# Kernel tuning notes

Measured on AMD Instinct MI355X. Metric: run time of the kernel, lower is better.

Reference implementation:

```python
import jax, jax.numpy as jnp
import numpy as np
import math

N_HEADS = 8

def setup_inputs() -> dict:
    key = jax.random.key(0)
    qkv = jax.random.normal(key, (2, 1536, 4096), dtype=jnp.float32)
    return {"qkv": qkv}

def reference(qkv):
    bs, width, length = qkv.shape
    ch = width // (3 * N_HEADS)
    # [bs*H, 3*ch, T] -> split into q, k, v each [bs*H, ch, T]
    qkv_r = qkv.reshape(bs * N_HEADS, 3 * ch, length)
    q, k, v = jnp.split(qkv_r, 3, axis=1)
    scale = 1.0 / math.sqrt(math.sqrt(ch))
    # scores [b, t, s]
    weight = jnp.einsum('bct,bcs->bts', q * scale, k * scale)
    weight = jax.nn.softmax(weight.astype(jnp.float32), axis=-1).astype(weight.dtype)
    a = jnp.einsum('bts,bcs->bct', weight, v)
    return a.reshape(bs, N_HEADS * ch, length)
```

## Files before the change

kernel.cpp:

```cpp
#include <hip/hip_runtime.h>

#define TSEQ 4096
#define QB   128
#define KB   64
#define NT   (TSEQ / KB)

typedef __attribute__((ext_vector_type(16))) float f32x16;
typedef __attribute__((ext_vector_type(8)))  short bf16x8;
typedef __attribute__((ext_vector_type(4)))  unsigned uint4v;

union Frag { unsigned u[4]; bf16x8 v; };

static __device__ __forceinline__ unsigned cvt_pk(float lo, float hi) {
  unsigned r;
  asm("v_cvt_pk_bf16_f32 %0, %1, %2" : "=v"(r) : "v"(lo), "v"(hi));
  return r;
}

static __device__ __forceinline__ void gload16(const void* g, void* l) {
  __builtin_amdgcn_global_load_lds(
      (const __attribute__((address_space(1))) unsigned*)g,
      (__attribute__((address_space(3))) unsigned*)l, 16, 0, 0);
}

__global__ __launch_bounds__(256)
void preconvert_kernel(const float* __restrict__ qkv,
                       unsigned short* __restrict__ kimg,
                       unsigned short* __restrict__ vimg) {
  const int tile = blockIdx.x & 63;
  const int bh   = blockIdx.x >> 6;
  const int bsI  = bh >> 3;
  const int head = bh & 7;
  const size_t base = ((size_t)bsI * 1536 + (size_t)head * 192) * TSEQ;
  const float* __restrict__ Kg = qkv + base + (size_t)64  * TSEQ;
  const float* __restrict__ Vg = qkv + base + (size_t)128 * TSEQ;
  const int s0 = tile * KB;
  const int t  = threadIdx.x;
  const size_t tb = (size_t)(bh * 64 + tile) * 8192;

  {
    const int s = t & 63;
    char* kout = (char*)kimg + tb + (size_t)s * 128;
    const unsigned swz = (unsigned)((s & 7) << 4);
#pragma unroll
    for (int q = 0; q < 2; ++q) {
      const int cc = (t >> 6) + q * 4;
      float f[8];
#pragma unroll
      for (int j = 0; j < 8; ++j)
        f[j] = Kg[(size_t)(8 * cc + j) * TSEQ + s0 + s];
      uint4v d = { cvt_pk(f[0], f[1]), cvt_pk(f[2], f[3]),
                   cvt_pk(f[4], f[5]), cvt_pk(f[6], f[7]) };
      *(uint4v*)(kout + (((unsigned)(cc << 4)) ^ swz)) = d;
    }
  }

  {
    const int c  = t >> 2;
    const int sb = (t & 3) * 16;
    const float* src = &Vg[(size_t)c * TSEQ + s0 + sb];
    const float4 a0 = ((const float4*)src)[0];
    const float4 a1 = ((const float4*)src)[1];
    const float4 a2 = ((const float4*)src)[2];
    const float4 a3 = ((const float4*)src)[3];
    char* vout = (char*)vimg + tb + (size_t)c * 128;
    const unsigned cswz = (unsigned)((c & 7) << 4);
    const int ss = (t & 3) * 2;
    uint4v d0 = { cvt_pk(a0.x, a0.y), cvt_pk(a0.z, a0.w),
                  cvt_pk(a1.x, a1.y), cvt_pk(a1.z, a1.w) };
    uint4v d1 = { cvt_pk(a2.x, a2.y), cvt_pk(a2.z, a2.w),
                  cvt_pk(a3.x, a3.y), cvt_pk(a3.z, a3.w) };
    *(uint4v*)(vout + (((unsigned)(ss << 4)) ^ cswz))       = d0;
    *(uint4v*)(vout + (((unsigned)((ss + 1) << 4)) ^ cswz)) = d1;
  }
}

__global__ __launch_bounds__(256, 2)
void qkv_attn_kernel(const float* __restrict__ qkv,
                     const unsigned short* __restrict__ kimg,
                     const unsigned short* __restrict__ vimg,
                     float* __restrict__ out) {
  __shared__ __align__(16) unsigned short Kt[2][KB * 64];
  __shared__ __align__(16) unsigned short Vt[2][64 * KB];

  const int tid  = threadIdx.x;
  const int w    = tid >> 6;
  const int lane = tid & 63;
  const int h    = lane >> 5;
  const int ln   = lane & 31;

  const int bid  = blockIdx.x;
  const int qt   = bid & 31;
  const int bh   = bid >> 5;
  const int bsI  = bh >> 3;
  const int head = bh & 7;

  const size_t base = ((size_t)bsI * 1536 + (size_t)head * 192) * TSEQ;
  const float* __restrict__ Qg = qkv + base;

  const int tq = qt * QB + w * 32 + ln;

  const float QSCALE = 0.125f * 1.44269504088896340736f;

  Frag qf[4];
#pragma unroll
  for (int ks = 0; ks < 4; ++ks) {
#pragma unroll
    for (int p = 0; p < 4; ++p) {
      const int c = ks * 16 + h * 8 + 2 * p;
      const float a = Qg[(size_t)c * TSEQ + tq] * QSCALE;
      const float b = Qg[(size_t)(c + 1) * TSEQ + tq] * QSCALE;
      qf[ks].u[p] = cvt_pk(a, b);
    }
  }

  f32x16 acc0 = {0,0,0,0,0,0,0,0,0,0,0,0,0,0,0,0};
  f32x16 acc1 = {0,0,0,0,0,0,0,0,0,0,0,0,0,0,0,0};
  float lrun = 0.0f;

  const size_t hb = (size_t)bh * 64 * 8192;
  const char* __restrict__ kim = (const char*)kimg + hb + w * 2048 + lane * 16;
  const char* __restrict__ vim = (const char*)vimg + hb + w * 2048 + lane * 16;

#define STAGE(buf, tile)                                                    \
  {                                                                         \
    const size_t o = (size_t)(tile) * 8192;                                 \
    char* kl = (char*)(&Kt[buf][0]) + w * 2048;                             \
    char* vl = (char*)(&Vt[buf][0]) + w * 2048;                             \
    gload16(kim + o, kl);                                                   \
    gload16(kim + o + 1024, kl + 1024);                                     \
    gload16(vim + o, vl);                                                   \
    gload16(vim + o + 1024, vl + 1024);                                     \
  }

  STAGE(0, 0);

  for (int it = 0; it < NT; ++it) {
    const int cur = it & 1;

    if (it + 1 < NT) {
      STAGE(cur ^ 1, it + 1);
      asm volatile("s_waitcnt vmcnt(4)" ::: "memory");
    } else {
      asm volatile("s_waitcnt vmcnt(0)" ::: "memory");
    }
    __builtin_amdgcn_s_barrier();
    __builtin_amdgcn_sched_barrier(0);

    const char* kbase = (const char*)(&Kt[cur][0]);
    const char* vbase = (const char*)(&Vt[cur][0]);

    f32x16 sc0 = {0,0,0,0,0,0,0,0,0,0,0,0,0,0,0,0};
    f32x16 sc1 = {0,0,0,0,0,0,0,0,0,0,0,0,0,0,0,0};
    __builtin_amdgcn_s_setprio(1);
#pragma unroll
    for (int ks = 0; ks < 4; ++ks) {
      const int coff2 = (ks * 16 + h * 8) * 2;
      const int sA = ln, sB = 32 + ln;
      const bf16x8 kA = *(const bf16x8*)(kbase + sA * 128 + (coff2 ^ ((sA & 7) << 4)));
      const bf16x8 kB = *(const bf16x8*)(kbase + sB * 128 + (coff2 ^ ((sB & 7) << 4)));
      sc0 = __builtin_amdgcn_mfma_f32_32x32x16_bf16(kA, qf[ks].v, sc0, 0, 0, 0);
      sc1 = __builtin_amdgcn_mfma_f32_32x32x16_bf16(kB, qf[ks].v, sc1, 0, 0, 0);
    }
    __builtin_amdgcn_s_setprio(0);

    float ssum = 0.0f;
#pragma unroll
    for (int r = 0; r < 16; ++r) {
      const float p0 = __builtin_amdgcn_exp2f(sc0[r]);
      const float p1 = __builtin_amdgcn_exp2f(sc1[r]);
      sc0[r] = p0; sc1[r] = p1;
      ssum += p0 + p1;
    }
    ssum += __shfl_xor(ssum, 32);
    lrun += ssum;

    Frag pf[4];
#pragma unroll
    for (int mt = 0; mt < 2; ++mt) {
      const f32x16& s = mt ? sc1 : sc0;
      unsigned A0 = cvt_pk(s[0],  s[1]),  A1 = cvt_pk(s[2],  s[3]);
      unsigned B0 = cvt_pk(s[4],  s[5]),  B1 = cvt_pk(s[6],  s[7]);
      unsigned C0 = cvt_pk(s[8],  s[9]),  C1 = cvt_pk(s[10], s[11]);
      unsigned D0 = cvt_pk(s[12], s[13]), D1 = cvt_pk(s[14], s[15]);
      asm("v_permlane32_swap_b32 %0, %1" : "+v"(A0), "+v"(B0));
      asm("v_permlane32_swap_b32 %0, %1" : "+v"(A1), "+v"(B1));
      asm("v_permlane32_swap_b32 %0, %1" : "+v"(C0), "+v"(D0));
      asm("v_permlane32_swap_b32 %0, %1" : "+v"(C1), "+v"(D1));
      pf[2 * mt + 0].u[0] = A0; pf[2 * mt + 0].u[1] = A1;
      pf[2 * mt + 0].u[2] = B0; pf[2 * mt + 0].u[3] = B1;
      pf[2 * mt + 1].u[0] = C0; pf[2 * mt + 1].u[1] = C1;
      pf[2 * mt + 1].u[2] = D0; pf[2 * mt + 1].u[3] = D1;
    }

    __builtin_amdgcn_s_setprio(1);
#pragma unroll
    for (int ks = 0; ks < 4; ++ks) {
      const int soff2 = (ks * 16 + h * 8) * 2;
      const int cA = ln, cB = 32 + ln;
      const bf16x8 vA = *(const bf16x8*)(vbase + cA * 128 + (soff2 ^ ((cA & 7) << 4)));
      const bf16x8 vB = *(const bf16x8*)(vbase + cB * 128 + (soff2 ^ ((cB & 7) << 4)));
      acc0 = __builtin_amdgcn_mfma_f32_32x32x16_bf16(vA, pf[ks].v, acc0, 0, 0, 0);
      acc1 = __builtin_amdgcn_mfma_f32_32x32x16_bf16(vB, pf[ks].v, acc1, 0, 0, 0);
    }
    __builtin_amdgcn_s_setprio(0);

    __builtin_amdgcn_sched_barrier(0);
    __builtin_amdgcn_s_barrier();
  }

  const float linv = 1.0f / lrun;
  const size_t obase = ((size_t)bsI * 512 + (size_t)head * 64) * TSEQ + tq;
#pragma unroll
  for (int r = 0; r < 16; ++r) {
    const int crow = (r & 3) + 8 * (r >> 2) + 4 * h;
    out[obase + (size_t)crow * TSEQ]        = acc0[r] * linv;
    out[obase + (size_t)(crow + 32) * TSEQ] = acc1[r] * linv;
  }
}

extern "C" void kernel_launch(void* const* d_in, const int* in_sizes, int n_in,
                              void* d_out, int out_size, void* d_ws, size_t ws_size,
                              hipStream_t stream) {
  const float* qkv = (const float*)d_in[0];
  float* out = (float*)d_out;
  (void)in_sizes; (void)n_in; (void)out_size; (void)ws_size;

  unsigned short* kimg = (unsigned short*)d_ws;
  unsigned short* vimg = (unsigned short*)((char*)d_ws + 8388608);

  hipLaunchKernelGGL(preconvert_kernel, dim3(16 * 64), dim3(256), 0, stream,
                     qkv, kimg, vimg);
  hipLaunchKernelGGL(qkv_attn_kernel, dim3(16 * (TSEQ / QB)), dim3(256), 0,
                     stream, qkv, kimg, vimg, out);
}
```

Measured before the change: 102.8 us.

## Double key tile to 128 and remap blocks so each head stays on one XCD

Raises the key/value tile from 64 to 128, which halves the main-loop iterations and their barriers and gives each wave four independent score MFMAs and eight PV MFMAs per tile. Both kernels now decode block IDs so that all blocks of a given batch-head land on the same XCD, keeping that head's K/V images in one L2. The K/V staging is also issued before the Q fragment loads, so the first tile fetch overlaps the Q conversion. In exchange, LDS use per block doubles and register pressure rises (four score accumulators and eight P fragments), which may limit the two-blocks-per-CU occupancy.

```diff
diff --git a/kernel.cpp b/kernel.cpp
--- a/kernel.cpp
+++ b/kernel.cpp
@@ -2,7 +2,7 @@
 
 #define TSEQ 4096
 #define QB   128
-#define KB   64
+#define KB   128
 #define NT   (TSEQ / KB)
 
 typedef __attribute__((ext_vector_type(16))) float f32x16;
@@ -23,12 +23,18 @@
       (__attribute__((address_space(3))) unsigned*)l, 16, 0, 0);
 }
 
+static __device__ __forceinline__ void decode_bid(int hw, int& bh, int& sub) {
+  const int xcd = hw & 7, slot = hw >> 3;
+  bh  = xcd * 2 + (slot >> 5);
+  sub = slot & 31;
+}
+
 __global__ __launch_bounds__(256)
 void preconvert_kernel(const float* __restrict__ qkv,
                        unsigned short* __restrict__ kimg,
                        unsigned short* __restrict__ vimg) {
-  const int tile = blockIdx.x & 63;
-  const int bh   = blockIdx.x >> 6;
+  int bh, tile;
+  decode_bid(blockIdx.x, bh, tile);
   const int bsI  = bh >> 3;
   const int head = bh & 7;
   const size_t base = ((size_t)bsI * 1536 + (size_t)head * 192) * TSEQ;
@@ -36,15 +42,15 @@
   const float* __restrict__ Vg = qkv + base + (size_t)128 * TSEQ;
   const int s0 = tile * KB;
   const int t  = threadIdx.x;
-  const size_t tb = (size_t)(bh * 64 + tile) * 8192;
+  const size_t tb = (size_t)(bh * NT + tile) * 16384;
 
   {
-    const int s = t & 63;
+    const int s = t & 127;
     char* kout = (char*)kimg + tb + (size_t)s * 128;
     const unsigned swz = (unsigned)((s & 7) << 4);
 #pragma unroll
-    for (int q = 0; q < 2; ++q) {
-      const int cc = (t >> 6) + q * 4;
+    for (int q = 0; q < 4; ++q) {
+      const int cc = (t >> 7) * 4 + q;
       float f[8];
 #pragma unroll
       for (int j = 0; j < 8; ++j)
@@ -56,22 +62,18 @@
   }
 
   {
-    const int c  = t >> 2;
-    const int sb = (t & 3) * 16;
-    const float* src = &Vg[(size_t)c * TSEQ + s0 + sb];
-    const float4 a0 = ((const float4*)src)[0];
-    const float4 a1 = ((const float4*)src)[1];
-    const float4 a2 = ((const float4*)src)[2];
-    const float4 a3 = ((const float4*)src)[3];
-    char* vout = (char*)vimg + tb + (size_t)c * 128;
+    const int c = t >> 2;
+    char* vout = (char*)vimg + tb + (size_t)c * 256;
     const unsigned cswz = (unsigned)((c & 7) << 4);
-    const int ss = (t & 3) * 2;
-    uint4v d0 = { cvt_pk(a0.x, a0.y), cvt_pk(a0.z, a0.w),
-                  cvt_pk(a1.x, a1.y), cvt_pk(a1.z, a1.w) };
-    uint4v d1 = { cvt_pk(a2.x, a2.y), cvt_pk(a2.z, a2.w),
-                  cvt_pk(a3.x, a3.y), cvt_pk(a3.z, a3.w) };
-    *(uint4v*)(vout + (((unsigned)(ss << 4)) ^ cswz))       = d0;
-    *(uint4v*)(vout + (((unsigned)((ss + 1) << 4)) ^ cswz)) = d1;
+#pragma unroll
+    for (int q = 0; q < 4; ++q) {
+      const int ss = (t & 3) * 4 + q;
+      const float4 a0 = ((const float4*)&Vg[(size_t)c * TSEQ + s0 + 8 * ss])[0];
+      const float4 a1 = ((const float4*)&Vg[(size_t)c * TSEQ + s0 + 8 * ss])[1];
+      uint4v d = { cvt_pk(a0.x, a0.y), cvt_pk(a0.z, a0.w),
+                   cvt_pk(a1.x, a1.y), cvt_pk(a1.z, a1.w) };
+      *(uint4v*)(vout + (((unsigned)(ss << 4)) ^ cswz)) = d;
+    }
   }
 }
 
@@ -89,9 +91,8 @@
   const int h    = lane >> 5;
   const int ln   = lane & 31;
 
-  const int bid  = blockIdx.x;
-  const int qt   = bid & 31;
-  const int bh   = bid >> 5;
+  int bh, qt;
+  decode_bid(blockIdx.x, bh, qt);
   const int bsI  = bh >> 3;
   const int head = bh & 7;
 
@@ -101,6 +102,27 @@
   const int tq = qt * QB + w * 32 + ln;
 
   const float QSCALE = 0.125f * 1.44269504088896340736f;
+
+  const size_t hb = (size_t)bh * NT * 16384;
+  const char* __restrict__ kim = (const char*)kimg + hb + w * 4096 + lane * 16;
+  const char* __restrict__ vim = (const char*)vimg + hb + w * 4096 + lane * 16;
+
+#define STAGE(buf, tile)                                                    \
+  {                                                                         \
+    const size_t o = (size_t)(tile) * 16384;                                \
+    char* kl = (char*)(&Kt[buf][0]) + w * 4096;                             \
+    char* vl = (char*)(&Vt[buf][0]) + w * 4096;                             \
+    gload16(kim + o,        kl);                                            \
+    gload16(kim + o + 1024, kl + 1024);                                     \
+    gload16(kim + o + 2048, kl + 2048);                                     \
+    gload16(kim + o + 3072, kl + 3072);                                     \
+    gload16(vim + o,        vl);                                            \
+    gload16(vim + o + 1024, vl + 1024);                                     \
+    gload16(vim + o + 2048, vl + 2048);                                     \
+    gload16(vim + o + 3072, vl + 3072);                                     \
+  }
+
+  STAGE(0, 0);
 
   Frag qf[4];
 #pragma unroll
@@ -118,29 +140,14 @@
   f32x16 acc1 = {0,0,0,0,0,0,0,0,0,0,0,0,0,0,0,0};
   float lrun = 0.0f;
 
-  const size_t hb = (size_t)bh * 64 * 8192;
-  const char* __restrict__ kim = (const char*)kimg + hb + w * 2048 + lane * 16;
-  const char* __restrict__ vim = (const char*)vimg + hb + w * 2048 + lane * 16;
-
-#define STAGE(buf, tile)                                                    \
-  {                                                                         \
-    const size_t o = (size_t)(tile) * 8192;                                 \
-    char* kl = (char*)(&Kt[buf][0]) + w * 2048;                             \
-    char* vl = (char*)(&Vt[buf][0]) + w * 2048;                             \
-    gload16(kim + o, kl);                                                   \
-    gload16(kim + o + 1024, kl + 1024);                                     \
-    gload16(vim + o, vl);                                                   \
-    gload16(vim + o + 1024, vl + 1024);                                     \
-  }
-
-  STAGE(0, 0);
+  const unsigned lswz = (unsigned)((ln & 7) << 4);
 
   for (int it = 0; it < NT; ++it) {
     const int cur = it & 1;
 
     if (it + 1 < NT) {
       STAGE(cur ^ 1, it + 1);
-      asm volatile("s_waitcnt vmcnt(4)" ::: "memory");
+      asm volatile("s_waitcnt vmcnt(8)" ::: "memory");
     } else {
       asm volatile("s_waitcnt vmcnt(0)" ::: "memory");
     }
@@ -150,35 +157,39 @@
     const char* kbase = (const char*)(&Kt[cur][0]);
     const char* vbase = (const char*)(&Vt[cur][0]);
 
-    f32x16 sc0 = {0,0,0,0,0,0,0,0,0,0,0,0,0,0,0,0};
-    f32x16 sc1 = {0,0,0,0,0,0,0,0,0,0,0,0,0,0,0,0};
+    f32x16 sc[4];
+#pragma unroll
+    for (int m = 0; m < 4; ++m) sc[m] = (f32x16){0,0,0,0,0,0,0,0,0,0,0,0,0,0,0,0};
     __builtin_amdgcn_s_setprio(1);
 #pragma unroll
     for (int ks = 0; ks < 4; ++ks) {
-      const int coff2 = (ks * 16 + h * 8) * 2;
-      const int sA = ln, sB = 32 + ln;
-      const bf16x8 kA = *(const bf16x8*)(kbase + sA * 128 + (coff2 ^ ((sA & 7) << 4)));
-      const bf16x8 kB = *(const bf16x8*)(kbase + sB * 128 + (coff2 ^ ((sB & 7) << 4)));
-      sc0 = __builtin_amdgcn_mfma_f32_32x32x16_bf16(kA, qf[ks].v, sc0, 0, 0, 0);
-      sc1 = __builtin_amdgcn_mfma_f32_32x32x16_bf16(kB, qf[ks].v, sc1, 0, 0, 0);
+      const unsigned coffx = ((unsigned)(32 * ks + 16 * h)) ^ lswz;
+#pragma unroll
+      for (int m = 0; m < 4; ++m) {
+        const int row = 32 * m + ln;
+        const bf16x8 kf = *(const bf16x8*)(kbase + row * 128 + coffx);
+        sc[m] = __builtin_amdgcn_mfma_f32_32x32x16_bf16(kf, qf[ks].v, sc[m], 0, 0, 0);
+      }
     }
     __builtin_amdgcn_s_setprio(0);
 
     float ssum = 0.0f;
 #pragma unroll
-    for (int r = 0; r < 16; ++r) {
-      const float p0 = __builtin_amdgcn_exp2f(sc0[r]);
-      const float p1 = __builtin_amdgcn_exp2f(sc1[r]);
-      sc0[r] = p0; sc1[r] = p1;
-      ssum += p0 + p1;
+    for (int m = 0; m < 4; ++m) {
+#pragma unroll
+      for (int r = 0; r < 16; ++r) {
+        const float p = __builtin_amdgcn_exp2f(sc[m][r]);
+        sc[m][r] = p;
+        ssum += p;
+      }
     }
     ssum += __shfl_xor(ssum, 32);
     lrun += ssum;
 
-    Frag pf[4];
-#pragma unroll
-    for (int mt = 0; mt < 2; ++mt) {
-      const f32x16& s = mt ? sc1 : sc0;
+    Frag pf[8];
+#pragma unroll
+    for (int m = 0; m < 4; ++m) {
+      const f32x16& s = sc[m];
       unsigned A0 = cvt_pk(s[0],  s[1]),  A1 = cvt_pk(s[2],  s[3]);
       unsigned B0 = cvt_pk(s[4],  s[5]),  B1 = cvt_pk(s[6],  s[7]);
       unsigned C0 = cvt_pk(s[8],  s[9]),  C1 = cvt_pk(s[10], s[11]);
@@ -187,19 +198,18 @@
       asm("v_permlane32_swap_b32 %0, %1" : "+v"(A1), "+v"(B1));
       asm("v_permlane32_swap_b32 %0, %1" : "+v"(C0), "+v"(D0));
       asm("v_permlane32_swap_b32 %0, %1" : "+v"(C1), "+v"(D1));
-      pf[2 * mt + 0].u[0] = A0; pf[2 * mt + 0].u[1] = A1;
-      pf[2 * mt + 0].u[2] = B0; pf[2 * mt + 0].u[3] = B1;
-      pf[2 * mt + 1].u[0] = C0; pf[2 * mt + 1].u[1] = C1;
-      pf[2 * mt + 1].u[2] = D0; pf[2 * mt + 1].u[3] = D1;
+      pf[2 * m + 0].u[0] = A0; pf[2 * m + 0].u[1] = A1;
+      pf[2 * m + 0].u[2] = B0; pf[2 * m + 0].u[3] = B1;
+      pf[2 * m + 1].u[0] = C0; pf[2 * m + 1].u[1] = C1;
+      pf[2 * m + 1].u[2] = D0; pf[2 * m + 1].u[3] = D1;
     }
 
     __builtin_amdgcn_s_setprio(1);
 #pragma unroll
-    for (int ks = 0; ks < 4; ++ks) {
-      const int soff2 = (ks * 16 + h * 8) * 2;
-      const int cA = ln, cB = 32 + ln;
-      const bf16x8 vA = *(const bf16x8*)(vbase + cA * 128 + (soff2 ^ ((cA & 7) << 4)));
-      const bf16x8 vB = *(const bf16x8*)(vbase + cB * 128 + (soff2 ^ ((cB & 7) << 4)));
+    for (int ks = 0; ks < 8; ++ks) {
+      const unsigned soffx = ((unsigned)(32 * ks + 16 * h)) ^ lswz;
+      const bf16x8 vA = *(const bf16x8*)(vbase + ln * 256 + soffx);
+      const bf16x8 vB = *(const bf16x8*)(vbase + (32 + ln) * 256 + soffx);
       acc0 = __builtin_amdgcn_mfma_f32_32x32x16_bf16(vA, pf[ks].v, acc0, 0, 0, 0);
       acc1 = __builtin_amdgcn_mfma_f32_32x32x16_bf16(vB, pf[ks].v, acc1, 0, 0, 0);
     }
@@ -229,7 +239,7 @@
   unsigned short* kimg = (unsigned short*)d_ws;
   unsigned short* vimg = (unsigned short*)((char*)d_ws + 8388608);
 
-  hipLaunchKernelGGL(preconvert_kernel, dim3(16 * 64), dim3(256), 0, stream,
+  hipLaunchKernelGGL(preconvert_kernel, dim3(16 * NT), dim3(256), 0, stream,
                      qkv, kimg, vimg);
   hipLaunchKernelGGL(qkv_attn_kernel, dim3(16 * (TSEQ / QB)), dim3(256), 0,
                      stream, qkv, kimg, vimg, out);
```

Result: faster. 99.52 us (-3.2%).

## Split key sequence across two wave groups per block and remap blocks per XCD

Applied to the files above, without the earlier changes.

Each attention block now has 512 threads in two groups of four waves. Each group walks half of the key/value tiles with its own double-buffered LDS slots, and at the end the partial accumulators and row sums are merged through LDS before writing. Block indices are remapped so that all blocks of one batch-head land on the same XCD, for both the preconvert and attention kernels, to improve L2 reuse of the bf16 K/V images. The aim is more waves in flight and a shorter serial loop per wave. The cost is a doubled LDS footprint per block, an extra reduction pass through shared memory, and half the threads idle during the output store.

```diff
diff --git a/kernel.cpp b/kernel.cpp
--- a/kernel.cpp
+++ b/kernel.cpp
@@ -3,7 +3,8 @@
 #define TSEQ 4096
 #define QB   128
 #define KB   64
-#define NT   (TSEQ / KB)
+#define NTT  (TSEQ / KB)
+#define NTG  (NTT / 2)
 
 typedef __attribute__((ext_vector_type(16))) float f32x16;
 typedef __attribute__((ext_vector_type(8)))  short bf16x8;
@@ -23,12 +24,23 @@
       (__attribute__((address_space(3))) unsigned*)l, 16, 0, 0);
 }
 
+static __device__ __forceinline__ void decode_attn(int hw, int& bh, int& sub) {
+  const int xcd = hw & 7, slot = hw >> 3;
+  bh  = xcd * 2 + (slot >> 5);
+  sub = slot & 31;
+}
+static __device__ __forceinline__ void decode_pre(int hw, int& bh, int& sub) {
+  const int xcd = hw & 7, slot = hw >> 3;
+  bh  = xcd * 2 + (slot >> 6);
+  sub = slot & 63;
+}
+
 __global__ __launch_bounds__(256)
 void preconvert_kernel(const float* __restrict__ qkv,
                        unsigned short* __restrict__ kimg,
                        unsigned short* __restrict__ vimg) {
-  const int tile = blockIdx.x & 63;
-  const int bh   = blockIdx.x >> 6;
+  int bh, tile;
+  decode_pre(blockIdx.x, bh, tile);
   const int bsI  = bh >> 3;
   const int head = bh & 7;
   const size_t base = ((size_t)bsI * 1536 + (size_t)head * 192) * TSEQ;
@@ -36,7 +48,7 @@
   const float* __restrict__ Vg = qkv + base + (size_t)128 * TSEQ;
   const int s0 = tile * KB;
   const int t  = threadIdx.x;
-  const size_t tb = (size_t)(bh * 64 + tile) * 8192;
+  const size_t tb = (size_t)(bh * NTT + tile) * 8192;
 
   {
     const int s = t & 63;
@@ -75,32 +87,50 @@
   }
 }
 
-__global__ __launch_bounds__(256, 2)
+__global__ __launch_bounds__(512, 4)
 void qkv_attn_kernel(const float* __restrict__ qkv,
                      const unsigned short* __restrict__ kimg,
                      const unsigned short* __restrict__ vimg,
                      float* __restrict__ out) {
-  __shared__ __align__(16) unsigned short Kt[2][KB * 64];
-  __shared__ __align__(16) unsigned short Vt[2][64 * KB];
+  __shared__ __align__(16) unsigned short Kt[2][2][KB * 64];
+  __shared__ __align__(16) unsigned short Vt[2][2][64 * KB];
 
   const int tid  = threadIdx.x;
   const int w    = tid >> 6;
+  const int g    = w >> 2;
+  const int wg   = w & 3;
   const int lane = tid & 63;
   const int h    = lane >> 5;
   const int ln   = lane & 31;
 
-  const int bid  = blockIdx.x;
-  const int qt   = bid & 31;
-  const int bh   = bid >> 5;
+  int bh, qt;
+  decode_attn(blockIdx.x, bh, qt);
   const int bsI  = bh >> 3;
   const int head = bh & 7;
 
   const size_t base = ((size_t)bsI * 1536 + (size_t)head * 192) * TSEQ;
   const float* __restrict__ Qg = qkv + base;
 
-  const int tq = qt * QB + w * 32 + ln;
+  const int tq = qt * QB + wg * 32 + ln;
 
   const float QSCALE = 0.125f * 1.44269504088896340736f;
+
+  const size_t hb = (size_t)bh * NTT * 8192;
+  const char* __restrict__ kim = (const char*)kimg + hb + wg * 2048 + lane * 16;
+  const char* __restrict__ vim = (const char*)vimg + hb + wg * 2048 + lane * 16;
+
+#define STAGE(buf, tile)                                                    \
+  {                                                                         \
+    const size_t o = (size_t)(g * NTG + (tile)) * 8192;                     \
+    char* kl = (char*)(&Kt[g][buf][0]) + wg * 2048;                         \
+    char* vl = (char*)(&Vt[g][buf][0]) + wg * 2048;                         \
+    gload16(kim + o, kl);                                                   \
+    gload16(kim + o + 1024, kl + 1024);                                    \
+    gload16(vim + o, vl);                                                   \
+    gload16(vim + o + 1024, vl + 1024);                                    \
+  }
+
+  STAGE(0, 0);
 
   Frag qf[4];
 #pragma unroll
@@ -118,27 +148,10 @@
   f32x16 acc1 = {0,0,0,0,0,0,0,0,0,0,0,0,0,0,0,0};
   float lrun = 0.0f;
 
-  const size_t hb = (size_t)bh * 64 * 8192;
-  const char* __restrict__ kim = (const char*)kimg + hb + w * 2048 + lane * 16;
-  const char* __restrict__ vim = (const char*)vimg + hb + w * 2048 + lane * 16;
-
-#define STAGE(buf, tile)                                                    \
-  {                                                                         \
-    const size_t o = (size_t)(tile) * 8192;                                 \
-    char* kl = (char*)(&Kt[buf][0]) + w * 2048;                             \
-    char* vl = (char*)(&Vt[buf][0]) + w * 2048;                             \
-    gload16(kim + o, kl);                                                   \
-    gload16(kim + o + 1024, kl + 1024);                                     \
-    gload16(vim + o, vl);                                                   \
-    gload16(vim + o + 1024, vl + 1024);                                     \
-  }
-
-  STAGE(0, 0);
-
-  for (int it = 0; it < NT; ++it) {
+  for (int it = 0; it < NTG; ++it) {
     const int cur = it & 1;
 
-    if (it + 1 < NT) {
+    if (it + 1 < NTG) {
       STAGE(cur ^ 1, it + 1);
       asm volatile("s_waitcnt vmcnt(4)" ::: "memory");
     } else {
@@ -147,8 +160,8 @@
     __builtin_amdgcn_s_barrier();
     __builtin_amdgcn_sched_barrier(0);
 
-    const char* kbase = (const char*)(&Kt[cur][0]);
-    const char* vbase = (const char*)(&Vt[cur][0]);
+    const char* kbase = (const char*)(&Kt[g][cur][0]);
+    const char* vbase = (const char*)(&Vt[g][cur][0]);
 
     f32x16 sc0 = {0,0,0,0,0,0,0,0,0,0,0,0,0,0,0,0};
     f32x16 sc1 = {0,0,0,0,0,0,0,0,0,0,0,0,0,0,0,0};
@@ -209,13 +222,31 @@
     __builtin_amdgcn_s_barrier();
   }
 
-  const float linv = 1.0f / lrun;
-  const size_t obase = ((size_t)bsI * 512 + (size_t)head * 64) * TSEQ + tq;
-#pragma unroll
-  for (int r = 0; r < 16; ++r) {
-    const int crow = (r & 3) + 8 * (r >> 2) + 4 * h;
-    out[obase + (size_t)crow * TSEQ]        = acc0[r] * linv;
-    out[obase + (size_t)(crow + 32) * TSEQ] = acc1[r] * linv;
+  float* exch0 = (float*)(&Kt[0][0][0]);
+  float* exch1 = (float*)(&Vt[0][0][0]);
+  float* lex   = (float*)((char*)(&Vt[0][0][0]) + 20480);
+  const int t0 = tid & 255;
+
+  if (g == 1) {
+#pragma unroll
+    for (int r = 0; r < 16; ++r) {
+      exch0[t0 * 17 + r] = acc0[r];
+      exch1[t0 * 17 + r] = acc1[r];
+    }
+    lex[t0] = lrun;
+  }
+  __syncthreads();
+  if (g == 0) {
+    const float linv = 1.0f / (lrun + lex[t0]);
+    const size_t obase = ((size_t)bsI * 512 + (size_t)head * 64) * TSEQ + tq;
+#pragma unroll
+    for (int r = 0; r < 16; ++r) {
+      const int crow = (r & 3) + 8 * (r >> 2) + 4 * h;
+      out[obase + (size_t)crow * TSEQ] =
+          (acc0[r] + exch0[t0 * 17 + r]) * linv;
+      out[obase + (size_t)(crow + 32) * TSEQ] =
+          (acc1[r] + exch1[t0 * 17 + r]) * linv;
+    }
   }
 }
 
@@ -229,8 +260,8 @@
   unsigned short* kimg = (unsigned short*)d_ws;
   unsigned short* vimg = (unsigned short*)((char*)d_ws + 8388608);
 
-  hipLaunchKernelGGL(preconvert_kernel, dim3(16 * 64), dim3(256), 0, stream,
+  hipLaunchKernelGGL(preconvert_kernel, dim3(16 * NTT), dim3(256), 0, stream,
                      qkv, kimg, vimg);
-  hipLaunchKernelGGL(qkv_attn_kernel, dim3(16 * (TSEQ / QB)), dim3(256), 0,
+  hipLaunchKernelGGL(qkv_attn_kernel, dim3(16 * (TSEQ / QB)), dim3(512), 0,
                      stream, qkv, kimg, vimg, out);
 }
```

Measured after the change: 94.41 us. 1.09x faster.

## Split keys across waves with per-wave LDS buffers and cross-wave reduction

Applied to the files above, without the earlier changes.

Each block now owns 64 queries instead of 128. Its four waves each take a quarter of the key range with private double-buffered LDS, so the per-iteration block barriers go away. Each wave computes two 32-query tiles that share every K/V fragment load, and the K/V images are re-tiled into 32-key chunks. At the end, partial accumulators and row sums are reduced through LDS. Block IDs are also remapped to group heads across XCDs. The trade-offs are more LDS use, a final reduction, twice as many blocks, and higher register pressure from four accumulators.

```diff
diff --git a/kernel.cpp b/kernel.cpp
--- a/kernel.cpp
+++ b/kernel.cpp
@@ -1,9 +1,6 @@
 #include <hip/hip_runtime.h>
 
 #define TSEQ 4096
-#define QB   128
-#define KB   64
-#define NT   (TSEQ / KB)
 
 typedef __attribute__((ext_vector_type(16))) float f32x16;
 typedef __attribute__((ext_vector_type(8)))  short bf16x8;
@@ -27,51 +24,40 @@
 void preconvert_kernel(const float* __restrict__ qkv,
                        unsigned short* __restrict__ kimg,
                        unsigned short* __restrict__ vimg) {
-  const int tile = blockIdx.x & 63;
-  const int bh   = blockIdx.x >> 6;
+  const int hw   = blockIdx.x;
+  const int slot = hw >> 3;
+  const int bh   = (hw & 7) * 2 + (slot >> 7);
+  const int tile = slot & 127;
   const int bsI  = bh >> 3;
   const int head = bh & 7;
   const size_t base = ((size_t)bsI * 1536 + (size_t)head * 192) * TSEQ;
   const float* __restrict__ Kg = qkv + base + (size_t)64  * TSEQ;
   const float* __restrict__ Vg = qkv + base + (size_t)128 * TSEQ;
-  const int s0 = tile * KB;
+  const int s0 = tile * 32;
   const int t  = threadIdx.x;
-  const size_t tb = (size_t)(bh * 64 + tile) * 8192;
+  const size_t tb = (size_t)(bh * 128 + tile) * 4096;
 
   {
-    const int s = t & 63;
-    char* kout = (char*)kimg + tb + (size_t)s * 128;
-    const unsigned swz = (unsigned)((s & 7) << 4);
-#pragma unroll
-    for (int q = 0; q < 2; ++q) {
-      const int cc = (t >> 6) + q * 4;
-      float f[8];
-#pragma unroll
-      for (int j = 0; j < 8; ++j)
-        f[j] = Kg[(size_t)(8 * cc + j) * TSEQ + s0 + s];
-      uint4v d = { cvt_pk(f[0], f[1]), cvt_pk(f[2], f[3]),
-                   cvt_pk(f[4], f[5]), cvt_pk(f[6], f[7]) };
-      *(uint4v*)(kout + (((unsigned)(cc << 4)) ^ swz)) = d;
-    }
+    const int s = t & 31, cc = t >> 5;
+    float f[8];
+#pragma unroll
+    for (int j = 0; j < 8; ++j)
+      f[j] = Kg[(size_t)(8 * cc + j) * TSEQ + s0 + s];
+    uint4v d = { cvt_pk(f[0], f[1]), cvt_pk(f[2], f[3]),
+                 cvt_pk(f[4], f[5]), cvt_pk(f[6], f[7]) };
+    *(uint4v*)((char*)kimg + tb + (size_t)s * 128 +
+               (((unsigned)(cc << 4)) ^ ((unsigned)((s & 7) << 4)))) = d;
   }
 
   {
-    const int c  = t >> 2;
-    const int sb = (t & 3) * 16;
-    const float* src = &Vg[(size_t)c * TSEQ + s0 + sb];
+    const int c = t >> 2, ss = t & 3;
+    const float* src = &Vg[(size_t)c * TSEQ + s0 + 8 * ss];
     const float4 a0 = ((const float4*)src)[0];
     const float4 a1 = ((const float4*)src)[1];
-    const float4 a2 = ((const float4*)src)[2];
-    const float4 a3 = ((const float4*)src)[3];
-    char* vout = (char*)vimg + tb + (size_t)c * 128;
-    const unsigned cswz = (unsigned)((c & 7) << 4);
-    const int ss = (t & 3) * 2;
-    uint4v d0 = { cvt_pk(a0.x, a0.y), cvt_pk(a0.z, a0.w),
-                  cvt_pk(a1.x, a1.y), cvt_pk(a1.z, a1.w) };
-    uint4v d1 = { cvt_pk(a2.x, a2.y), cvt_pk(a2.z, a2.w),
-                  cvt_pk(a3.x, a3.y), cvt_pk(a3.z, a3.w) };
-    *(uint4v*)(vout + (((unsigned)(ss << 4)) ^ cswz))       = d0;
-    *(uint4v*)(vout + (((unsigned)((ss + 1) << 4)) ^ cswz)) = d1;
+    uint4v d = { cvt_pk(a0.x, a0.y), cvt_pk(a0.z, a0.w),
+                 cvt_pk(a1.x, a1.y), cvt_pk(a1.z, a1.w) };
+    *(uint4v*)((char*)vimg + tb + (size_t)c * 64 +
+               (((unsigned)(ss << 4)) ^ ((unsigned)((c & 3) << 4)))) = d;
   }
 }
 
@@ -80,8 +66,7 @@
                      const unsigned short* __restrict__ kimg,
                      const unsigned short* __restrict__ vimg,
                      float* __restrict__ out) {
-  __shared__ __align__(16) unsigned short Kt[2][KB * 64];
-  __shared__ __align__(16) unsigned short Vt[2][64 * KB];
+  __shared__ __align__(16) char lds[65536];
 
   const int tid  = threadIdx.x;
   const int w    = tid >> 6;
@@ -89,96 +74,118 @@
   const int h    = lane >> 5;
   const int ln   = lane & 31;
 
-  const int bid  = blockIdx.x;
-  const int qt   = bid & 31;
-  const int bh   = bid >> 5;
-  const int bsI  = bh >> 3;
-  const int head = bh & 7;
+  const int hw    = blockIdx.x;
+  const int slot  = hw >> 3;
+  const int bh    = (hw & 7) * 2 + (slot >> 6);
+  const int qslot = slot & 63;
+  const int bsI   = bh >> 3;
+  const int head  = bh & 7;
 
   const size_t base = ((size_t)bsI * 1536 + (size_t)head * 192) * TSEQ;
   const float* __restrict__ Qg = qkv + base;
-
-  const int tq = qt * QB + w * 32 + ln;
+  const int q0 = qslot * 64;
 
   const float QSCALE = 0.125f * 1.44269504088896340736f;
 
-  Frag qf[4];
+  char* kbuf0 = lds + w * 16384;
+  char* kbuf1 = kbuf0 + 4096;
+  char* vbuf0 = kbuf0 + 8192;
+  char* vbuf1 = kbuf0 + 12288;
+
+  const char* kim = (const char*)kimg + ((size_t)bh * 128 + w * 32) * 4096 + lane * 16;
+  const char* vim = (const char*)vimg + ((size_t)bh * 128 + w * 32) * 4096 + lane * 16;
+
+#define STAGE(kb, vb, it)                                                   \
+  {                                                                         \
+    const char* ks_ = kim + (size_t)(it) * 4096;                            \
+    const char* vs_ = vim + (size_t)(it) * 4096;                            \
+    gload16(ks_,        kb);                                                \
+    gload16(ks_ + 1024, (char*)(kb) + 1024);                                \
+    gload16(ks_ + 2048, (char*)(kb) + 2048);                                \
+    gload16(ks_ + 3072, (char*)(kb) + 3072);                                \
+    gload16(vs_,        vb);                                                \
+    gload16(vs_ + 1024, (char*)(vb) + 1024);                                \
+    gload16(vs_ + 2048, (char*)(vb) + 2048);                                \
+    gload16(vs_ + 3072, (char*)(vb) + 3072);                                \
+  }
+
+  STAGE(kbuf0, vbuf0, 0);
+
+  Frag qf0[4], qf1[4];
 #pragma unroll
   for (int ks = 0; ks < 4; ++ks) {
 #pragma unroll
     for (int p = 0; p < 4; ++p) {
       const int c = ks * 16 + h * 8 + 2 * p;
-      const float a = Qg[(size_t)c * TSEQ + tq] * QSCALE;
-      const float b = Qg[(size_t)(c + 1) * TSEQ + tq] * QSCALE;
-      qf[ks].u[p] = cvt_pk(a, b);
-    }
-  }
-
-  f32x16 acc0 = {0,0,0,0,0,0,0,0,0,0,0,0,0,0,0,0};
-  f32x16 acc1 = {0,0,0,0,0,0,0,0,0,0,0,0,0,0,0,0};
-  float lrun = 0.0f;
-
-  const size_t hb = (size_t)bh * 64 * 8192;
-  const char* __restrict__ kim = (const char*)kimg + hb + w * 2048 + lane * 16;
-  const char* __restrict__ vim = (const char*)vimg + hb + w * 2048 + lane * 16;
-
-#define STAGE(buf, tile)                                                    \
-  {                                                                         \
-    const size_t o = (size_t)(tile) * 8192;                                 \
-    char* kl = (char*)(&Kt[buf][0]) + w * 2048;                             \
-    char* vl = (char*)(&Vt[buf][0]) + w * 2048;                             \
-    gload16(kim + o, kl);                                                   \
-    gload16(kim + o + 1024, kl + 1024);                                     \
-    gload16(vim + o, vl);                                                   \
-    gload16(vim + o + 1024, vl + 1024);                                     \
-  }
-
-  STAGE(0, 0);
-
-  for (int it = 0; it < NT; ++it) {
+      const float a0 = Qg[(size_t)c * TSEQ + q0 + ln] * QSCALE;
+      const float b0 = Qg[(size_t)(c + 1) * TSEQ + q0 + ln] * QSCALE;
+      const float a1 = Qg[(size_t)c * TSEQ + q0 + 32 + ln] * QSCALE;
+      const float b1 = Qg[(size_t)(c + 1) * TSEQ + q0 + 32 + ln] * QSCALE;
+      qf0[ks].u[p] = cvt_pk(a0, b0);
+      qf1[ks].u[p] = cvt_pk(a1, b1);
+    }
+  }
+
+  int koff[4], voff[2][2];
+#pragma unroll
+  for (int ks = 0; ks < 4; ++ks) {
+    const int off2 = (ks * 16 + h * 8) * 2;
+    koff[ks] = ln * 128 + (off2 ^ ((ln & 7) << 4));
+  }
+#pragma unroll
+  for (int ks2 = 0; ks2 < 2; ++ks2) {
+    const int ss = ks2 * 2 + h;
+    voff[ks2][0] = ln * 64        + (((unsigned)(ss << 4)) ^ ((ln & 3) << 4));
+    voff[ks2][1] = (32 + ln) * 64 + (((unsigned)(ss << 4)) ^ ((ln & 3) << 4));
+  }
+
+  f32x16 zv = {0,0,0,0,0,0,0,0,0,0,0,0,0,0,0,0};
+  asm("" : "+v"(zv));
+
+  f32x16 acc00 = zv, acc01 = zv, acc10 = zv, acc11 = zv;
+  float lr0 = 0.0f, lr1 = 0.0f;
+
+  for (int it = 0; it < 32; ++it) {
     const int cur = it & 1;
-
-    if (it + 1 < NT) {
-      STAGE(cur ^ 1, it + 1);
-      asm volatile("s_waitcnt vmcnt(4)" ::: "memory");
+    char* kb = cur ? kbuf1 : kbuf0;
+    char* vb = cur ? vbuf1 : vbuf0;
+
+    if (it + 1 < 32) {
+      STAGE(cur ? kbuf0 : kbuf1, cur ? vbuf0 : vbuf1, it + 1);
+      asm volatile("s_waitcnt vmcnt(8)" ::: "memory");
     } else {
       asm volatile("s_waitcnt vmcnt(0)" ::: "memory");
     }
-    __builtin_amdgcn_s_barrier();
     __builtin_amdgcn_sched_barrier(0);
 
-    const char* kbase = (const char*)(&Kt[cur][0]);
-    const char* vbase = (const char*)(&Vt[cur][0]);
-
-    f32x16 sc0 = {0,0,0,0,0,0,0,0,0,0,0,0,0,0,0,0};
-    f32x16 sc1 = {0,0,0,0,0,0,0,0,0,0,0,0,0,0,0,0};
-    __builtin_amdgcn_s_setprio(1);
-#pragma unroll
-    for (int ks = 0; ks < 4; ++ks) {
-      const int coff2 = (ks * 16 + h * 8) * 2;
-      const int sA = ln, sB = 32 + ln;
-      const bf16x8 kA = *(const bf16x8*)(kbase + sA * 128 + (coff2 ^ ((sA & 7) << 4)));
-      const bf16x8 kB = *(const bf16x8*)(kbase + sB * 128 + (coff2 ^ ((sB & 7) << 4)));
-      sc0 = __builtin_amdgcn_mfma_f32_32x32x16_bf16(kA, qf[ks].v, sc0, 0, 0, 0);
-      sc1 = __builtin_amdgcn_mfma_f32_32x32x16_bf16(kB, qf[ks].v, sc1, 0, 0, 0);
-    }
-    __builtin_amdgcn_s_setprio(0);
-
-    float ssum = 0.0f;
+    f32x16 sc0, sc1;
+    {
+      const bf16x8 kA = *(const bf16x8*)(kb + koff[0]);
+      sc0 = __builtin_amdgcn_mfma_f32_32x32x16_bf16(kA, qf0[0].v, zv, 0, 0, 0);
+      sc1 = __builtin_amdgcn_mfma_f32_32x32x16_bf16(kA, qf1[0].v, zv, 0, 0, 0);
+    }
+#pragma unroll
+    for (int ks = 1; ks < 4; ++ks) {
+      const bf16x8 kA = *(const bf16x8*)(kb + koff[ks]);
+      sc0 = __builtin_amdgcn_mfma_f32_32x32x16_bf16(kA, qf0[ks].v, sc0, 0, 0, 0);
+      sc1 = __builtin_amdgcn_mfma_f32_32x32x16_bf16(kA, qf1[ks].v, sc1, 0, 0, 0);
+    }
+
+    float ls0 = 0.0f, ls1 = 0.0f;
 #pragma unroll
     for (int r = 0; r < 16; ++r) {
       const float p0 = __builtin_amdgcn_exp2f(sc0[r]);
       const float p1 = __builtin_amdgcn_exp2f(sc1[r]);
       sc0[r] = p0; sc1[r] = p1;
-      ssum += p0 + p1;
-    }
-    ssum += __shfl_xor(ssum, 32);
-    lrun += ssum;
-
-    Frag pf[4];
-#pragma unroll
-    for (int mt = 0; mt < 2; ++mt) {
-      const f32x16& s = mt ? sc1 : sc0;
+      ls0 += p0; ls1 += p1;
+    }
+    lr0 += ls0; lr1 += ls1;
+
+    Frag pf0[2], pf1[2];
+#pragma unroll
+    for (int nb = 0; nb < 2; ++nb) {
+      const f32x16& s = nb ? sc1 : sc0;
+      Frag* pf = nb ? pf1 : pf0;
       unsigned A0 = cvt_pk(s[0],  s[1]),  A1 = cvt_pk(s[2],  s[3]);
       unsigned B0 = cvt_pk(s[4],  s[5]),  B1 = cvt_pk(s[6],  s[7]);
       unsigned C0 = cvt_pk(s[8],  s[9]),  C1 = cvt_pk(s[10], s[11]);
@@ -187,35 +194,60 @@
       asm("v_permlane32_swap_b32 %0, %1" : "+v"(A1), "+v"(B1));
       asm("v_permlane32_swap_b32 %0, %1" : "+v"(C0), "+v"(D0));
       asm("v_permlane32_swap_b32 %0, %1" : "+v"(C1), "+v"(D1));
-      pf[2 * mt + 0].u[0] = A0; pf[2 * mt + 0].u[1] = A1;
-      pf[2 * mt + 0].u[2] = B0; pf[2 * mt + 0].u[3] = B1;
-      pf[2 * mt + 1].u[0] = C0; pf[2 * mt + 1].u[1] = C1;
-      pf[2 * mt + 1].u[2] = D0; pf[2 * mt + 1].u[3] = D1;
-    }
-
-    __builtin_amdgcn_s_setprio(1);
-#pragma unroll
-    for (int ks = 0; ks < 4; ++ks) {
-      const int soff2 = (ks * 16 + h * 8) * 2;
-      const int cA = ln, cB = 32 + ln;
-      const bf16x8 vA = *(const bf16x8*)(vbase + cA * 128 + (soff2 ^ ((cA & 7) << 4)));
-      const bf16x8 vB = *(const bf16x8*)(vbase + cB * 128 + (soff2 ^ ((cB & 7) << 4)));
-      acc0 = __builtin_amdgcn_mfma_f32_32x32x16_bf16(vA, pf[ks].v, acc0, 0, 0, 0);
-      acc1 = __builtin_amdgcn_mfma_f32_32x32x16_bf16(vB, pf[ks].v, acc1, 0, 0, 0);
-    }
-    __builtin_amdgcn_s_setprio(0);
+      pf[0].u[0] = A0; pf[0].u[1] = A1; pf[0].u[2] = B0; pf[0].u[3] = B1;
+      pf[1].u[0] = C0; pf[1].u[1] = C1; pf[1].u[2] = D0; pf[1].u[3] = D1;
+    }
+
+#pragma unroll
+    for (int ks2 = 0; ks2 < 2; ++ks2) {
+      const bf16x8 vA = *(const bf16x8*)(vb + voff[ks2][0]);
+      const bf16x8 vB = *(const bf16x8*)(vb + voff[ks2][1]);
+      acc00 = __builtin_amdgcn_mfma_f32_32x32x16_bf16(vA, pf0[ks2].v, acc00, 0, 0, 0);
+      acc01 = __builtin_amdgcn_mfma_f32_32x32x16_bf16(vA, pf1[ks2].v, acc01, 0, 0, 0);
+      acc10 = __builtin_amdgcn_mfma_f32_32x32x16_bf16(vB, pf0[ks2].v, acc10, 0, 0, 0);
+      acc11 = __builtin_amdgcn_mfma_f32_32x32x16_bf16(vB, pf1[ks2].v, acc11, 0, 0, 0);
+    }
 
     __builtin_amdgcn_sched_barrier(0);
-    __builtin_amdgcn_s_barrier();
-  }
-
-  const float linv = 1.0f / lrun;
-  const size_t obase = ((size_t)bsI * 512 + (size_t)head * 64) * TSEQ + tq;
-#pragma unroll
-  for (int r = 0; r < 16; ++r) {
-    const int crow = (r & 3) + 8 * (r >> 2) + 4 * h;
-    out[obase + (size_t)crow * TSEQ]        = acc0[r] * linv;
-    out[obase + (size_t)(crow + 32) * TSEQ] = acc1[r] * linv;
+  }
+
+  lr0 += __shfl_xor(lr0, 32);
+  lr1 += __shfl_xor(lr1, 32);
+
+  __syncthreads();
+  float* ex = (float*)lds;
+  if (w > 0) {
+    float* p = ex + (size_t)((w - 1) * 64 + lane) * 66;
+#pragma unroll
+    for (int r = 0; r < 16; ++r) {
+      p[r]      = acc00[r];
+      p[16 + r] = acc01[r];
+      p[32 + r] = acc10[r];
+      p[48 + r] = acc11[r];
+    }
+    p[64] = lr0;
+    p[65] = lr1;
+  }
+  __syncthreads();
+  if (w == 0) {
+    const float* p0 = ex + (size_t)lane * 66;
+    const float* p1 = ex + (size_t)(64 + lane) * 66;
+    const float* p2 = ex + (size_t)(128 + lane) * 66;
+    const float linv0 = 1.0f / (lr0 + p0[64] + p1[64] + p2[64]);
+    const float linv1 = 1.0f / (lr1 + p0[65] + p1[65] + p2[65]);
+    const size_t obase = ((size_t)bsI * 512 + (size_t)head * 64) * TSEQ + q0 + ln;
+#pragma unroll
+    for (int r = 0; r < 16; ++r) {
+      const int crow = (r & 3) + 8 * (r >> 2) + 4 * h;
+      const float a00 = acc00[r] + p0[r]      + p1[r]      + p2[r];
+      const float a01 = acc01[r] + p0[16 + r] + p1[16 + r] + p2[16 + r];
+      const float a10 = acc10[r] + p0[32 + r] + p1[32 + r] + p2[32 + r];
+      const float a11 = acc11[r] + p0[48 + r] + p1[48 + r] + p2[48 + r];
+      out[obase + (size_t)crow * TSEQ]             = a00 * linv0;
+      out[obase + (size_t)crow * TSEQ + 32]        = a01 * linv1;
+      out[obase + (size_t)(crow + 32) * TSEQ]      = a10 * linv0;
+      out[obase + (size_t)(crow + 32) * TSEQ + 32] = a11 * linv1;
+    }
   }
 }
 
@@ -229,8 +261,8 @@
   unsigned short* kimg = (unsigned short*)d_ws;
   unsigned short* vimg = (unsigned short*)((char*)d_ws + 8388608);
 
-  hipLaunchKernelGGL(preconvert_kernel, dim3(16 * 64), dim3(256), 0, stream,
+  hipLaunchKernelGGL(preconvert_kernel, dim3(2048), dim3(256), 0, stream,
                      qkv, kimg, vimg);
-  hipLaunchKernelGGL(qkv_attn_kernel, dim3(16 * (TSEQ / QB)), dim3(256), 0,
-                     stream, qkv, kimg, vimg, out);
-}
+  hipLaunchKernelGGL(qkv_attn_kernel, dim3(1024), dim3(256), 0, stream,
+                     qkv, kimg, vimg, out);
+}
```

Result: faster. 98.74 us (-4.0%).
